# Kernel optimization log

Measured on AMD Instinct MI355X. Metric: run time of the kernel, lower is better.

## Reference

```python
import jax, jax.numpy as jnp
import numpy as np

N = 2048
IN_FEAT = 256
OUT_FEAT = 64
E_FEAT = 32
NHID = 64
ALPHA = 0.2
NHEADS = 4
NLAYERS = 3
NEG_INF = -9e15


def setup_inputs() -> dict:
    key = jax.random.key(0)
    ks = jax.random.split(key, 6)
    x = jax.random.normal(ks[0], (N, IN_FEAT), dtype=jnp.float32)
    adj = jax.random.randint(ks[1], (N, N), 0, 2, dtype=jnp.int32)
    e = jax.random.normal(ks[2], (N, N, E_FEAT), dtype=jnp.float32)
    # All layers share shapes because in_feat == nhid*nheads and out_feat == nhid.
    # xavier-ish scale
    W_e = jax.random.normal(ks[3], (NLAYERS, NHEADS, E_FEAT, IN_FEAT), dtype=jnp.float32) * (1.414 * (2.0 / (E_FEAT + IN_FEAT)) ** 0.5)
    W = jax.random.normal(ks[4], (NLAYERS, NHEADS, IN_FEAT, NHID), dtype=jnp.float32) * (1.414 * (2.0 / (IN_FEAT + NHID)) ** 0.5)
    a = jax.random.normal(ks[5], (NLAYERS, NHEADS, 3 * NHID), dtype=jnp.float32) * (1.414 * (2.0 / (3 * NHID + 1)) ** 0.5)
    return {"x": x, "adj": adj, "e": e, "W_e": W_e, "W": W, "a": a}


def reference(x, adj, e, W_e, W, a):
    # dropout = 0.0 / eval mode -> identity
    out = W.shape[-1]
    nlayers = W.shape[0]
    mask = (adj > 0)[None]  # [1, N, N], broadcast over heads
    for l in range(nlayers):
        islast = (l == nlayers - 1)
        h = jnp.einsum('ni,hio->hno', x, W[l])  # [H, N, out]
        a1 = a[l, :, :out]            # [H, out]
        a2 = a[l, :, out:2 * out]     # [H, out]
        a3 = a[l, :, 2 * out:]        # [H, out]
        # score_ij = leakyrelu(a1.h_i + a2.h_j + a3.(e_ij @ W_e @ W))
        coef = jnp.einsum('heo,ho->he', jnp.einsum('hei,hio->heo', W_e[l], W[l]), a3)  # [H, E_FEAT]
        e_score = jnp.einsum('nmf,hf->hnm', e, coef)  # [H, N, N]
        s1 = jnp.einsum('hno,ho->hn', h, a1)[:, :, None]
        s2 = jnp.einsum('hno,ho->hn', h, a2)[:, None, :]
        score = jax.nn.leaky_relu(s1 + s2 + e_score, ALPHA)
        att = jax.nn.softmax(jnp.where(mask, score, NEG_INF), axis=-1)
        h_prime = jnp.einsum('hnm,hmo->hno', att, h)  # [H, N, out]
        if islast:
            x = jax.nn.elu(h_prime.mean(axis=0))  # [N, out]
        else:
            # concat heads along feature dim (head-major), with per-head elu
            x = jnp.transpose(jax.nn.elu(h_prime), (1, 0, 2)).reshape(h_prime.shape[1], -1)
    return x
```

## Files before the change

kernel.cpp:

```cpp
#include <hip/hip_runtime.h>
#include <cstdint>
#include <cstddef>

#define Nn 2048
#define FIN 256
#define EFEAT 32
#define HID 64
#define NH 4
#define NL 3
#define LRELU_A 0.2f

typedef _Float16 h4 __attribute__((ext_vector_type(4)));
typedef _Float16 h8 __attribute__((ext_vector_type(8)));
typedef float f4 __attribute__((ext_vector_type(4)));

#define NEGH ((_Float16)(-60000.0f))

__global__ void k_coef(const float* __restrict__ W, const float* __restrict__ We,
                       const float* __restrict__ a, float* __restrict__ coef) {
  int lh = blockIdx.x;
  int t = threadIdx.x;
  __shared__ float tl[FIN];
  const float* Wb = W + (size_t)lh * FIN * HID;
  const float* ab = a + (size_t)lh * (3 * HID) + 2 * HID;
  float acc = 0.f;
#pragma unroll 8
  for (int o = 0; o < HID; ++o) acc = fmaf(Wb[(size_t)t * HID + o], ab[o], acc);
  tl[t] = acc;
  __syncthreads();
  if (t < EFEAT) {
    const float* Web = We + ((size_t)lh * EFEAT + t) * FIN;
    float c = 0.f;
    for (int i = 0; i < FIN; ++i) c = fmaf(Web[i], tl[i], c);
    coef[lh * EFEAT + t] = c;
  }
}

template <int C>
__global__ __launch_bounds__(256) void k_escore(
    const float* __restrict__ e, const int* __restrict__ adj,
    const float* __restrict__ coef, _Float16* __restrict__ es) {
  size_t idx = (size_t)blockIdx.x * 256 + threadIdx.x;
  int m = (int)(idx & (Nn - 1));
  int n = (int)(idx >> 11);
  int mt = m >> 6, ml = m & 63;
  const size_t cstride = (size_t)32 * Nn * 64;
  size_t sbase = ((size_t)mt * Nn + n) * 64 + (size_t)ml;
  int aj = adj[idx];
  float evv[EFEAT] = {};
  if (aj != 0) {
    const float4* ep = (const float4*)(e + idx * EFEAT);
#pragma unroll
    for (int g = 0; g < 8; ++g) {
      float4 v = ep[g];
      evv[g * 4 + 0] = v.x; evv[g * 4 + 1] = v.y; evv[g * 4 + 2] = v.z; evv[g * 4 + 3] = v.w;
    }
  }
#pragma clang loop unroll(disable)
  for (int c = 0; c < C; ++c) {
    const float* cf = coef + c * EFEAT;
    float acc = 0.f;
#pragma unroll
    for (int f = 0; f < EFEAT; ++f) acc = fmaf(evv[f], cf[f], acc);
    es[(size_t)c * cstride + sbase] = aj ? (_Float16)acc : NEGH;
  }
}

__global__ __launch_bounds__(256) void k_h(
    const float* __restrict__ x, const float* __restrict__ W,
    const float* __restrict__ a, int layer,
    _Float16* __restrict__ hT, float* __restrict__ s1, float* __restrict__ s2) {
  int t = threadIdx.x;
  int n0 = blockIdx.x * 8;
  int h = t >> 6, o = t & 63;
  const float* Wb = W + ((size_t)(layer * NH + h) * FIN) * HID + o;
  const float* xb = x + (size_t)n0 * FIN;
  float acc[8] = {};
  for (int i0 = 0; i0 < FIN; i0 += 4) {
    float w0 = Wb[(size_t)(i0 + 0) * HID];
    float w1 = Wb[(size_t)(i0 + 1) * HID];
    float w2 = Wb[(size_t)(i0 + 2) * HID];
    float w3 = Wb[(size_t)(i0 + 3) * HID];
#pragma unroll
    for (int j = 0; j < 8; ++j) {
      float4 xv = *(const float4*)(xb + (size_t)j * FIN + i0);
      acc[j] = fmaf(xv.x, w0, acc[j]);
      acc[j] = fmaf(xv.y, w1, acc[j]);
      acc[j] = fmaf(xv.z, w2, acc[j]);
      acc[j] = fmaf(xv.w, w3, acc[j]);
    }
  }
  const float* ab = a + (size_t)(layer * NH + h) * (3 * HID);
  float a1v = ab[o], a2v = ab[HID + o];
#pragma unroll
  for (int j = 0; j < 8; ++j) {
    float r1 = acc[j] * a1v, r2 = acc[j] * a2v;
#pragma unroll
    for (int d = 1; d < 64; d <<= 1) {
      r1 += __shfl_xor(r1, d, 64);
      r2 += __shfl_xor(r2, d, 64);
    }
    if (o == 0) { s1[h * Nn + n0 + j] = r1; s2[h * Nn + n0 + j] = r2; }
  }
  int mt = n0 >> 6, ml = n0 & 63;
  h8 hv;
#pragma unroll
  for (int j = 0; j < 8; ++j) hv[j] = (_Float16)acc[j];
  *(h8*)(hT + (((size_t)h * 32 + mt) * 64 + o) * 64 + ml) = hv;
}

__global__ __launch_bounds__(512) void k_attn(
    const _Float16* __restrict__ es, const _Float16* __restrict__ hT,
    const float* __restrict__ s1, const float* __restrict__ s2,
    float* __restrict__ hp, float* __restrict__ xn, int layer, int last) {
  int h = blockIdx.x;
  int n0 = blockIdx.y * 16;
  int t = threadIdx.x;
  int w = t >> 6;
  int l = t & 63;
  int col = l & 15, grp = l >> 4;
  int n = n0 + col;
  float s1v = s1[h * Nn + n];
  const _Float16* esb = es + (size_t)(layer * NH + h) * ((size_t)32 * Nn * 64);
  const _Float16* hTb = hT + (size_t)h * ((size_t)32 * 64 * 64);
  const float* s2b = s2 + h * Nn;

  float M = -3.0e38f, S = 0.f;
  f4 acc[4] = {};

  for (int c16 = 0; c16 < 16; ++c16) {
    int m0 = w * 256 + c16 * 16;
    int mt = m0 >> 6;
    int ml0 = (m0 & 63) + grp * 4;
    h4 ev = *(const h4*)(esb + ((size_t)mt * Nn + n) * 64 + ml0);
    float4 sv = *(const float4*)(s2b + m0 + grp * 4);
    float sc0 = s1v + sv.x + (float)ev[0]; sc0 = fmaxf(sc0, LRELU_A * sc0);
    float sc1 = s1v + sv.y + (float)ev[1]; sc1 = fmaxf(sc1, LRELU_A * sc1);
    float sc2 = s1v + sv.z + (float)ev[2]; sc2 = fmaxf(sc2, LRELU_A * sc2);
    float sc3 = s1v + sv.w + (float)ev[3]; sc3 = fmaxf(sc3, LRELU_A * sc3);
    float cm = fmaxf(fmaxf(sc0, sc1), fmaxf(sc2, sc3));
    cm = fmaxf(cm, __shfl_xor(cm, 16, 64));
    cm = fmaxf(cm, __shfl_xor(cm, 32, 64));
    if (__any(cm > M)) {
      float Mn = fmaxf(M, cm);
      float fac = __expf(M - Mn);
      M = Mn;
      S *= fac;
#pragma unroll
      for (int ot = 0; ot < 4; ++ot) acc[ot] *= fac;
    }
    h4 pb;
    pb[0] = (_Float16)__expf(sc0 - M);
    pb[1] = (_Float16)__expf(sc1 - M);
    pb[2] = (_Float16)__expf(sc2 - M);
    pb[3] = (_Float16)__expf(sc3 - M);
    S += (float)pb[0] + (float)pb[1] + (float)pb[2] + (float)pb[3];
    const _Float16* hp0 = hTb + ((size_t)mt * 64 + col) * 64 + ml0;
#pragma unroll
    for (int ot = 0; ot < 4; ++ot) {
      h4 af = *(const h4*)(hp0 + (size_t)ot * 16 * 64);
      acc[ot] = __builtin_amdgcn_mfma_f32_16x16x16f16(af, pb, acc[ot], 0, 0, 0);
    }
  }

  S += __shfl_xor(S, 16, 64);
  S += __shfl_xor(S, 32, 64);

  __shared__ float red[8][16][64];
  __shared__ float Mw[8][16];
  __shared__ float Sw[8][16];
  if (l < 16) { Mw[w][l] = M; Sw[w][l] = S; }
#pragma unroll
  for (int ot = 0; ot < 4; ++ot)
    *(f4*)&red[w][col][ot * 16 + grp * 4] = acc[ot];
  __syncthreads();

  if (t < 256) {
    int nl = t >> 4, o0 = (t & 15) * 4;
    float Ms = Mw[0][nl];
#pragma unroll
    for (int ww = 1; ww < 8; ++ww) Ms = fmaxf(Ms, Mw[ww][nl]);
    float Ssum = 0.f;
    f4 v = {};
#pragma unroll
    for (int ww = 0; ww < 8; ++ww) {
      float f = __expf(Mw[ww][nl] - Ms);
      Ssum = fmaf(Sw[ww][nl], f, Ssum);
      f4 r = *(const f4*)&red[ww][nl][o0];
      v += r * f;
    }
    float is = 1.0f / Ssum;
    v *= is;
    if (last) {
      *(f4*)(hp + ((size_t)h * Nn + n0 + nl) * HID + o0) = v;
    } else {
      f4 xo;
#pragma unroll
      for (int k = 0; k < 4; ++k) xo[k] = v[k] > 0.f ? v[k] : expm1f(v[k]);
      *(f4*)(xn + (size_t)(n0 + nl) * FIN + h * HID + o0) = xo;
    }
  }
}

__global__ void k_out(const float* __restrict__ hp, float* __restrict__ out) {
  int idx = blockIdx.x * 256 + threadIdx.x;
  int n = idx >> 6, o = idx & 63;
  size_t b = (size_t)n * HID + o;
  float v = 0.25f * (hp[b] + hp[(size_t)Nn * HID + b] +
                     hp[2 * (size_t)Nn * HID + b] + hp[3 * (size_t)Nn * HID + b]);
  out[idx] = v > 0.f ? v : expm1f(v);
}

extern "C" void kernel_launch(void* const* d_in, const int* in_sizes, int n_in,
                              void* d_out, int out_size, void* d_ws, size_t ws_size,
                              hipStream_t stream) {
  const float* x_in = (const float*)d_in[0];
  const int* adj = (const int*)d_in[1];
  const float* e = (const float*)d_in[2];
  const float* We = (const float*)d_in[3];
  const float* W = (const float*)d_in[4];
  const float* a = (const float*)d_in[5];
  float* out = (float*)d_out;

  char* ws = (char*)d_ws;
  size_t off = 0;
  auto alloc = [&](size_t bytes) -> void* {
    off = (off + 255) & ~(size_t)255;
    void* p = ws + off;
    off += bytes;
    return p;
  };
  float* coef = (float*)alloc((size_t)NL * NH * EFEAT * sizeof(float));
  float* s1 = (float*)alloc((size_t)NH * Nn * sizeof(float));
  float* s2 = (float*)alloc((size_t)NH * Nn * sizeof(float));
  float* hp = (float*)alloc((size_t)NH * Nn * HID * sizeof(float));
  float* xA = (float*)alloc((size_t)Nn * FIN * sizeof(float));
  float* xB = (float*)alloc((size_t)Nn * FIN * sizeof(float));
  _Float16* hT = (_Float16*)alloc((size_t)NH * 32 * 64 * 64 * sizeof(_Float16));
  _Float16* es = (_Float16*)alloc((size_t)NL * NH * 32 * Nn * 64 * sizeof(_Float16));

  hipLaunchKernelGGL(k_coef, dim3(NL * NH), dim3(256), 0, stream, W, We, a, coef);

  size_t total = (size_t)Nn * Nn;
  hipLaunchKernelGGL((k_escore<NL * NH>), dim3((unsigned)(total / 256)), dim3(256), 0, stream,
                     e, adj, coef, es);

  for (int l = 0; l < NL; ++l) {
    const float* xcur = (l == 0) ? x_in : ((l == 1) ? xA : xB);
    float* xn = (l == 0) ? xA : xB;
    hipLaunchKernelGGL(k_h, dim3(Nn / 8), dim3(256), 0, stream, xcur, W, a, l, hT, s1, s2);
    hipLaunchKernelGGL(k_attn, dim3(NH, Nn / 16), dim3(512), 0, stream,
                       es, hT, s1, s2, hp, xn, l, l == NL - 1 ? 1 : 0);
  }
  hipLaunchKernelGGL(k_out, dim3(Nn * HID / 256), dim3(256), 0, stream, hp, out);
}
```

Measured before the change: 311.3 us.

## Use two-pass softmax in attention and halve rows per block in projection

```diff
diff --git a/kernel.cpp b/kernel.cpp
--- a/kernel.cpp
+++ b/kernel.cpp
@@ -71,18 +71,18 @@
     const float* __restrict__ a, int layer,
     _Float16* __restrict__ hT, float* __restrict__ s1, float* __restrict__ s2) {
   int t = threadIdx.x;
-  int n0 = blockIdx.x * 8;
+  int n0 = blockIdx.x * 4;
   int h = t >> 6, o = t & 63;
   const float* Wb = W + ((size_t)(layer * NH + h) * FIN) * HID + o;
   const float* xb = x + (size_t)n0 * FIN;
-  float acc[8] = {};
+  float acc[4] = {};
   for (int i0 = 0; i0 < FIN; i0 += 4) {
     float w0 = Wb[(size_t)(i0 + 0) * HID];
     float w1 = Wb[(size_t)(i0 + 1) * HID];
     float w2 = Wb[(size_t)(i0 + 2) * HID];
     float w3 = Wb[(size_t)(i0 + 3) * HID];
 #pragma unroll
-    for (int j = 0; j < 8; ++j) {
+    for (int j = 0; j < 4; ++j) {
       float4 xv = *(const float4*)(xb + (size_t)j * FIN + i0);
       acc[j] = fmaf(xv.x, w0, acc[j]);
       acc[j] = fmaf(xv.y, w1, acc[j]);
@@ -93,7 +93,7 @@
   const float* ab = a + (size_t)(layer * NH + h) * (3 * HID);
   float a1v = ab[o], a2v = ab[HID + o];
 #pragma unroll
-  for (int j = 0; j < 8; ++j) {
+  for (int j = 0; j < 4; ++j) {
     float r1 = acc[j] * a1v, r2 = acc[j] * a2v;
 #pragma unroll
     for (int d = 1; d < 64; d <<= 1) {
@@ -103,13 +103,13 @@
     if (o == 0) { s1[h * Nn + n0 + j] = r1; s2[h * Nn + n0 + j] = r2; }
   }
   int mt = n0 >> 6, ml = n0 & 63;
-  h8 hv;
-#pragma unroll
-  for (int j = 0; j < 8; ++j) hv[j] = (_Float16)acc[j];
-  *(h8*)(hT + (((size_t)h * 32 + mt) * 64 + o) * 64 + ml) = hv;
-}
-
-__global__ __launch_bounds__(512) void k_attn(
+  h4 hv;
+#pragma unroll
+  for (int j = 0; j < 4; ++j) hv[j] = (_Float16)acc[j];
+  *(h4*)(hT + (((size_t)h * 32 + mt) * 64 + o) * 64 + ml) = hv;
+}
+
+__global__ __launch_bounds__(512, 2) void k_attn(
     const _Float16* __restrict__ es, const _Float16* __restrict__ hT,
     const float* __restrict__ s1, const float* __restrict__ s2,
     float* __restrict__ hp, float* __restrict__ xn, int layer, int last) {
@@ -125,9 +125,9 @@
   const _Float16* hTb = hT + (size_t)h * ((size_t)32 * 64 * 64);
   const float* s2b = s2 + h * Nn;
 
-  float M = -3.0e38f, S = 0.f;
-  f4 acc[4] = {};
-
+  h4 sc16[16];
+  float pmax = -3.0e38f;
+#pragma unroll
   for (int c16 = 0; c16 < 16; ++c16) {
     int m0 = w * 256 + c16 * 16;
     int mt = m0 >> 6;
@@ -138,23 +138,31 @@
     float sc1 = s1v + sv.y + (float)ev[1]; sc1 = fmaxf(sc1, LRELU_A * sc1);
     float sc2 = s1v + sv.z + (float)ev[2]; sc2 = fmaxf(sc2, LRELU_A * sc2);
     float sc3 = s1v + sv.w + (float)ev[3]; sc3 = fmaxf(sc3, LRELU_A * sc3);
-    float cm = fmaxf(fmaxf(sc0, sc1), fmaxf(sc2, sc3));
-    cm = fmaxf(cm, __shfl_xor(cm, 16, 64));
-    cm = fmaxf(cm, __shfl_xor(cm, 32, 64));
-    if (__any(cm > M)) {
-      float Mn = fmaxf(M, cm);
-      float fac = __expf(M - Mn);
-      M = Mn;
-      S *= fac;
-#pragma unroll
-      for (int ot = 0; ot < 4; ++ot) acc[ot] *= fac;
-    }
+    h4 sch;
+    sch[0] = (_Float16)sc0; sch[1] = (_Float16)sc1;
+    sch[2] = (_Float16)sc2; sch[3] = (_Float16)sc3;
+    sc16[c16] = sch;
+    pmax = fmaxf(pmax, fmaxf(fmaxf(sc0, sc1), fmaxf(sc2, sc3)));
+  }
+  pmax = fmaxf(pmax, __shfl_xor(pmax, 16, 64));
+  float M = fmaxf(pmax, __shfl_xor(pmax, 32, 64));
+
+  float S = 0.f;
+  f4 acc[4] = {};
+#pragma unroll
+  for (int c16 = 0; c16 < 16; ++c16) {
+    int m0 = w * 256 + c16 * 16;
+    int mt = m0 >> 6;
+    int ml0 = (m0 & 63) + grp * 4;
+    h4 scv = sc16[c16];
+    float p0 = __expf((float)scv[0] - M);
+    float p1 = __expf((float)scv[1] - M);
+    float p2 = __expf((float)scv[2] - M);
+    float p3 = __expf((float)scv[3] - M);
+    S += p0 + p1 + p2 + p3;
     h4 pb;
-    pb[0] = (_Float16)__expf(sc0 - M);
-    pb[1] = (_Float16)__expf(sc1 - M);
-    pb[2] = (_Float16)__expf(sc2 - M);
-    pb[3] = (_Float16)__expf(sc3 - M);
-    S += (float)pb[0] + (float)pb[1] + (float)pb[2] + (float)pb[3];
+    pb[0] = (_Float16)p0; pb[1] = (_Float16)p1;
+    pb[2] = (_Float16)p2; pb[3] = (_Float16)p3;
     const _Float16* hp0 = hTb + ((size_t)mt * 64 + col) * 64 + ml0;
 #pragma unroll
     for (int ot = 0; ot < 4; ++ot) {
@@ -162,7 +170,6 @@
       acc[ot] = __builtin_amdgcn_mfma_f32_16x16x16f16(af, pb, acc[ot], 0, 0, 0);
     }
   }
-
   S += __shfl_xor(S, 16, 64);
   S += __shfl_xor(S, 32, 64);
 
@@ -248,7 +255,7 @@
   for (int l = 0; l < NL; ++l) {
     const float* xcur = (l == 0) ? x_in : ((l == 1) ? xA : xB);
     float* xn = (l == 0) ? xA : xB;
-    hipLaunchKernelGGL(k_h, dim3(Nn / 8), dim3(256), 0, stream, xcur, W, a, l, hT, s1, s2);
+    hipLaunchKernelGGL(k_h, dim3(Nn / 4), dim3(256), 0, stream, xcur, W, a, l, hT, s1, s2);
     hipLaunchKernelGGL(k_attn, dim3(NH, Nn / 16), dim3(512), 0, stream,
                        es, hT, s1, s2, hp, xn, l, l == NL - 1 ? 1 : 0);
   }
```

Result: faster. 259.6 us (-16.6%).
